# Kernel optimization log

Measured on AMD Instinct MI355X. Metric: run time of the kernel, lower is better.

Reference implementation:

```python
import jax, jax.numpy as jnp
import numpy as np

B, S, D, N = 4, 4096, 512, 512  # d_state must equal d_model for the original broadcast to be valid


def setup_inputs() -> dict:
    key = jax.random.key(0)
    ks = jax.random.split(key, 8)
    inv = 1.0 / np.sqrt(D)
    return {
        "x": jax.random.normal(ks[0], (B, S, D), dtype=jnp.float32),
        "state0": jnp.zeros((B, N), dtype=jnp.float32),
        "W_gate": (jax.random.normal(ks[1], (D, D)) * inv).astype(jnp.float32),  # x_proj_gate.weight [out,in]
        "b_gate": jnp.zeros((D,), jnp.float32),
        "W_sp": (jax.random.normal(ks[2], (N, D)) * inv).astype(jnp.float32),    # state_proj.weight [d_state, d_model]
        "b_sp": jnp.zeros((N,), jnp.float32),
        "W_out": (jax.random.normal(ks[3], (D, D)) * inv).astype(jnp.float32),   # out_proj.weight
        "b_out": jnp.zeros((D,), jnp.float32),
        "A_log": (jax.random.normal(ks[4], (D, N)) * 0.02).astype(jnp.float32),
        "D_param": jnp.ones((D,), jnp.float32),
    }


def reference(x, state0, W_gate, b_gate, W_sp, b_sp, W_out, b_out, A_log, D_param):
    # x_gate = silu(x_proj_gate(x))  [B,S,D]
    x_gate = jax.nn.silu(x @ W_gate.T + b_gate)
    # s = state_proj(x_gate)  [B,S,N]
    s = x_gate @ W_sp.T + b_sp
    # A = -exp(A_log); per-step decay = exp(mean_N(A))  [D] (== N by construction)
    A = -jnp.exp(A_log)
    decay = jnp.exp(A.mean(axis=-1))

    def step(state, s_t):  # state [B,N], s_t [B,N]
        state = state * decay + s_t
        return state, state

    state_f, states = jax.lax.scan(step, state0, jnp.swapaxes(s, 0, 1))  # states [S,B,N]
    # y_t = state_t @ state_proj.weight + D * u_t
    y = jnp.einsum('sbn,nd->bsd', states, W_sp) + D_param * x_gate
    out = y @ W_out.T + b_out  # out_proj
    return out, state_f
```

## Files before the change

kernel.cpp:

```cpp
#include <hip/hip_runtime.h>
#include <hip/hip_bf16.h>
#include <stdint.h>


typedef __bf16 bf16_t;
typedef bf16_t bf16x8 __attribute__((ext_vector_type(8)));
typedef bf16_t bf16x4 __attribute__((ext_vector_type(4)));
typedef float  f32x4  __attribute__((ext_vector_type(4)));

static __device__ __forceinline__ void async_copy16(bf16_t* lds, const bf16_t* g) {
    __builtin_amdgcn_global_load_lds((const __attribute__((address_space(1))) void*)g,
                                     (__attribute__((address_space(3))) void*)lds, 16, 0, 0);
}

template <int MODE, int NT>
__global__ __launch_bounds__(256, 2) void gemm_2ph(
    const bf16_t* __restrict__ A0, const bf16_t* __restrict__ W0,
    const bf16_t* __restrict__ A1, const bf16_t* __restrict__ W1,
    const float* __restrict__ bias, void* __restrict__ outp, int M)
{
    constexpr int K = 512;
    __shared__ bf16_t As[2][128 * 64];
    __shared__ bf16_t Bs[2][128 * 64];
    const int tid = threadIdx.x;
    int bid = blockIdx.x;
    {
        int nwg = gridDim.x;
        if ((nwg & 7) == 0) bid = (bid & 7) * (nwg >> 3) + (bid >> 3);
    }
    const int m0 = (bid >> 2) << 7, n0 = (bid & 3) << 7;
    const int l = tid & 63, w = tid >> 6;
    const int wr = w >> 1, wc = w & 1;
    const int lr = l & 15, kc = l >> 4;
    const int rloc = l >> 3, sc = (l & 7) ^ rloc;

    float bv[4];
    #pragma unroll
    for (int j = 0; j < 4; ++j)
        bv[j] = bias ? bias[n0 + wc * 64 + j * 16 + lr] : 0.f;

    f32x4 acc[4][4];
    const f32x4 z = {0.f, 0.f, 0.f, 0.f};
    #pragma unroll
    for (int i = 0; i < 4; ++i)
        #pragma unroll
        for (int j = 0; j < 4; ++j) acc[i][j] = z;

    auto stage = [&](int t) {
        const bf16_t* __restrict__ Asrc = (t < 8) ? A0 : A1;
        const bf16_t* __restrict__ Wsrc = (t < 8) ? W0 : W1;
        const int kk = (t & 7) << 6;
        bf16_t* bufA = As[t & 1];
        bf16_t* bufB = Bs[t & 1];
        #pragma unroll
        for (int v = 0; v < 4; ++v) {
            const int win = w * 4 + v;
            async_copy16(bufA + win * 512,
                         Asrc + (size_t)(m0 + win * 8 + rloc) * K + kk + sc * 8);
            async_copy16(bufB + win * 512,
                         Wsrc + (size_t)(n0 + win * 8 + rloc) * K + kk + sc * 8);
        }
    };

    stage(0);
    __syncthreads();

    #pragma unroll
    for (int t = 0; t < NT; ++t) {
        if (t + 1 < NT) stage(t + 1);
        const bf16_t* __restrict__ bufA = As[t & 1];
        const bf16_t* __restrict__ bufB = Bs[t & 1];
        bf16x8 a[2][4], b[2][4];
        #pragma unroll
        for (int ks = 0; ks < 2; ++ks) {
            #pragma unroll
            for (int i = 0; i < 4; ++i)
                a[ks][i] = *(const bf16x8*)(bufA + (wr * 64 + i * 16 + lr) * 64
                                            + (((ks * 4 + kc) ^ (lr & 7)) << 3));
            #pragma unroll
            for (int j = 0; j < 4; ++j)
                b[ks][j] = *(const bf16x8*)(bufB + (wc * 64 + j * 16 + lr) * 64
                                            + (((ks * 4 + kc) ^ (lr & 7)) << 3));
        }
        #pragma unroll
        for (int ks = 0; ks < 2; ++ks)
            #pragma unroll
            for (int i = 0; i < 4; ++i)
                #pragma unroll
                for (int j = 0; j < 4; ++j)
                    acc[i][j] = __builtin_amdgcn_mfma_f32_16x16x32_bf16(
                        a[ks][i], b[ks][j], acc[i][j], 0, 0, 0);
        if (t + 1 < NT) __syncthreads();
    }

    if (MODE == 0) {
        float* outF = (float*)outp;
        #pragma unroll
        for (int i = 0; i < 4; ++i) {
            const int row = m0 + wr * 64 + i * 16 + kc * 4;
            #pragma unroll
            for (int j = 0; j < 4; ++j) {
                const int col = n0 + wc * 64 + j * 16 + lr;
                #pragma unroll
                for (int r = 0; r < 4; ++r)
                    outF[(size_t)(row + r) * 512 + col] = acc[i][j][r] + bv[j];
            }
        }
    } else {
        __syncthreads();
        bf16_t* eps = &As[0][0];
        #pragma unroll
        for (int i = 0; i < 4; ++i) {
            const int row = wr * 64 + i * 16 + kc * 4;
            #pragma unroll
            for (int j = 0; j < 4; ++j) {
                const int col = wc * 64 + j * 16 + lr;
                #pragma unroll
                for (int r = 0; r < 4; ++r) {
                    float v = acc[i][j][r] + bv[j];
                    if (MODE == 2) v = v / (1.f + __expf(-v));
                    eps[(row + r) * 128 + col] = (bf16_t)v;
                }
            }
        }
        __syncthreads();
        bf16_t* outB = (bf16_t*)outp;
        #pragma unroll
        for (int s2 = 0; s2 < 8; ++s2) {
            const int row = s2 * 16 + (tid >> 4);
            const int col = (tid & 15) * 8;
            *(bf16x8*)(outB + (size_t)(m0 + row) * 512 + n0 + col) =
                *(const bf16x8*)(eps + row * 128 + col);
        }
    }
}

__global__ void prep_all(const float4* __restrict__ x, bf16x4* __restrict__ xb,
                         const float* __restrict__ Wg, const float* __restrict__ Wsp,
                         const float* __restrict__ Wo, const float* __restrict__ Dp,
                         bf16_t* __restrict__ Wg_bf, bf16_t* __restrict__ Wsp_bf,
                         bf16_t* __restrict__ Wo_bf, bf16_t* __restrict__ W2_bf,
                         const float* __restrict__ A_log, float* __restrict__ decay)
{
    const int blk = blockIdx.x, tid = threadIdx.x;
    {
        int i = blk * 256 + tid;
        float4 v = x[i];
        bf16x4 o;
        o[0] = (bf16_t)v.x; o[1] = (bf16_t)v.y; o[2] = (bf16_t)v.z; o[3] = (bf16_t)v.w;
        xb[i] = o;
    }
    if (blk < 1024) {
        int i = blk * 256 + tid;
        Wg_bf[i]  = (bf16_t)Wg[i];
        Wsp_bf[i] = (bf16_t)Wsp[i];
        float wo  = Wo[i];
        Wo_bf[i]  = (bf16_t)wo;
        W2_bf[i]  = (bf16_t)(wo * Dp[i & 511]);
    }
    if (blk < 128) {
        int d = blk * 4 + (tid >> 6);
        int ll = tid & 63;
        const float* row = A_log + (size_t)d * 512;
        float s = 0.f;
        for (int k = ll; k < 512; k += 64) s += expf(row[k]);
        #pragma unroll
        for (int off = 32; off > 0; off >>= 1) s += __shfl_down(s, off);
        if (ll == 0) decay[d] = expf(-s * (1.f / 512.f));
    }
}

__global__ void scan_partial(const bf16_t* __restrict__ s, const float* __restrict__ decay,
                             float* __restrict__ carry)
{
    int g = blockIdx.x * 256 + threadIdx.x;
    int n = g & 511, ch = (g >> 9) & 63, b = g >> 15;
    float dec = decay[n];
    const bf16_t* sp = s + (size_t)(b * 4096 + ch * 64) * 512 + n;
    float st = 0.f;
    #pragma unroll 8
    for (int i = 0; i < 64; ++i) st = st * dec + (float)sp[(size_t)i * 512];
    carry[(size_t)(b * 64 + ch) * 512 + n] = st;
}

__global__ void scan_carry(const float* __restrict__ carry, const float* __restrict__ decay,
                           const float* __restrict__ state0,
                           float* __restrict__ exc, float* __restrict__ state_f)
{
    int g = blockIdx.x * 256 + threadIdx.x;
    int n = g & 511, b = g >> 9;
    float dec = decay[n];
    float d64 = dec;
    #pragma unroll
    for (int t = 0; t < 6; ++t) d64 *= d64;
    float st = state0[g];
    for (int ch = 0; ch < 64; ++ch) {
        size_t idx = (size_t)(b * 64 + ch) * 512 + n;
        exc[idx] = st;
        st = st * d64 + carry[idx];
    }
    state_f[g] = st;
}

__global__ void scan_final(const bf16_t* __restrict__ s, const float* __restrict__ decay,
                           const float* __restrict__ exc, bf16_t* __restrict__ states)
{
    int g = blockIdx.x * 256 + threadIdx.x;
    int n = g & 511, ch = (g >> 9) & 63, b = g >> 15;
    float dec = decay[n];
    float st = exc[(size_t)(b * 64 + ch) * 512 + n];
    size_t base = (size_t)(b * 4096 + ch * 64) * 512 + n;
    #pragma unroll 8
    for (int i = 0; i < 64; ++i) {
        st = st * dec + (float)s[base + (size_t)i * 512];
        states[base + (size_t)i * 512] = (bf16_t)st;
    }
}

extern "C" void kernel_launch(void* const* d_in, const int* in_sizes, int n_in,
                              void* d_out, int out_size, void* d_ws, size_t ws_size,
                              hipStream_t stream)
{
    const float* x      = (const float*)d_in[0];
    const float* state0 = (const float*)d_in[1];
    const float* W_gate = (const float*)d_in[2];
    const float* b_gate = (const float*)d_in[3];
    const float* W_sp   = (const float*)d_in[4];
    const float* b_sp   = (const float*)d_in[5];
    const float* W_out  = (const float*)d_in[6];
    const float* b_out  = (const float*)d_in[7];
    const float* A_log  = (const float*)d_in[8];
    const float* D_par  = (const float*)d_in[9];
    float* out = (float*)d_out;

    char* ws = (char*)d_ws;
    bf16_t* x_bf   = (bf16_t*)ws;
    bf16_t* states = x_bf;
    bf16_t* xg_bf  = (bf16_t*)(ws + (16u << 20));
    bf16_t* s_bf   = (bf16_t*)(ws + (32u << 20));
    bf16_t* Wg_bf  = (bf16_t*)(ws + (48u << 20));
    bf16_t* Wsp_bf = Wg_bf + 262144;
    bf16_t* Wo_bf  = Wg_bf + 2 * 262144;
    bf16_t* W2_bf  = Wg_bf + 3 * 262144;
    bf16_t* WcT_bf = Wg_bf + 4 * 262144;
    float*  carry  = (float*)(Wg_bf + 5 * 262144);
    float*  exc    = carry + 131072;
    float*  decay  = exc + 131072;

    prep_all<<<dim3(8192), dim3(256), 0, stream>>>(
        (const float4*)x, (bf16x4*)x_bf, W_gate, W_sp, W_out, D_par,
        Wg_bf, Wsp_bf, Wo_bf, W2_bf, A_log, decay);

    gemm_2ph<1, 8><<<dim3(16), dim3(256), 0, stream>>>(
        Wo_bf, Wsp_bf, (const bf16_t*)nullptr, (const bf16_t*)nullptr,
        (const float*)nullptr, (void*)WcT_bf, 512);
    gemm_2ph<2, 8><<<dim3(512), dim3(256), 0, stream>>>(
        x_bf, Wg_bf, (const bf16_t*)nullptr, (const bf16_t*)nullptr,
        b_gate, (void*)xg_bf, 16384);
    gemm_2ph<1, 8><<<dim3(512), dim3(256), 0, stream>>>(
        xg_bf, Wsp_bf, (const bf16_t*)nullptr, (const bf16_t*)nullptr,
        b_sp, (void*)s_bf, 16384);

    scan_partial<<<dim3(512), dim3(256), 0, stream>>>(s_bf, decay, carry);
    scan_carry<<<dim3(8), dim3(256), 0, stream>>>(carry, decay, state0, exc, out + 8388608);
    scan_final<<<dim3(512), dim3(256), 0, stream>>>(s_bf, decay, exc, states);

    gemm_2ph<0, 16><<<dim3(512), dim3(256), 0, stream>>>(
        states, WcT_bf, xg_bf, W2_bf, b_out, (void*)out, 16384);
}
```

Baseline: 96.69 us.

## Fuse chunk-carry scan into state-proj GEMM epilogue and merge carry propagation

The state-projection GEMM now computes each 64-row chunk's partial scan carry directly from its LDS epilogue tile, which removes the separate scan_partial pass that re-read s from global memory. The carry-propagation kernel is dropped: each thread of the final scan replays the previous chunk carries itself, then writes the states and, for the last chunk, the final state. This saves two launches and a full read of s. In exchange the GEMM epilogue gets a serial 64-step loop and the final scan does up to 63 redundant carry steps per thread.

```diff
diff --git a/kernel.cpp b/kernel.cpp
--- a/kernel.cpp
+++ b/kernel.cpp
@@ -13,11 +13,12 @@
                                      (__attribute__((address_space(3))) void*)lds, 16, 0, 0);
 }
 
-template <int MODE, int NT>
+template <int MODE, int NT, bool SCAN>
 __global__ __launch_bounds__(256, 2) void gemm_2ph(
     const bf16_t* __restrict__ A0, const bf16_t* __restrict__ W0,
     const bf16_t* __restrict__ A1, const bf16_t* __restrict__ W1,
-    const float* __restrict__ bias, void* __restrict__ outp, int M)
+    const float* __restrict__ bias, void* __restrict__ outp,
+    const float* __restrict__ decay_g, float* __restrict__ carry_g)
 {
     constexpr int K = 512;
     __shared__ bf16_t As[2][128 * 64];
@@ -132,6 +133,16 @@
             *(bf16x8*)(outB + (size_t)(m0 + row) * 512 + n0 + col) =
                 *(const bf16x8*)(eps + row * 128 + col);
         }
+        if (SCAN) {
+            const int chalf = tid >> 7, col = tid & 127;
+            const int n = n0 + col;
+            const float dec = decay_g[n];
+            float st = 0.f;
+            #pragma unroll 8
+            for (int i = 0; i < 64; ++i)
+                st = st * dec + (float)eps[(chalf * 64 + i) * 128 + col];
+            carry_g[(size_t)((m0 >> 6) + chalf) * 512 + n] = st;
+        }
     }
 }
 
@@ -170,51 +181,27 @@
     }
 }
 
-__global__ void scan_partial(const bf16_t* __restrict__ s, const float* __restrict__ decay,
-                             float* __restrict__ carry)
+__global__ void scan_final2(const bf16_t* __restrict__ s, const float* __restrict__ decay,
+                            const float* __restrict__ carry, const float* __restrict__ state0,
+                            bf16_t* __restrict__ states, float* __restrict__ state_f)
 {
     int g = blockIdx.x * 256 + threadIdx.x;
     int n = g & 511, ch = (g >> 9) & 63, b = g >> 15;
     float dec = decay[n];
-    const bf16_t* sp = s + (size_t)(b * 4096 + ch * 64) * 512 + n;
-    float st = 0.f;
-    #pragma unroll 8
-    for (int i = 0; i < 64; ++i) st = st * dec + (float)sp[(size_t)i * 512];
-    carry[(size_t)(b * 64 + ch) * 512 + n] = st;
-}
-
-__global__ void scan_carry(const float* __restrict__ carry, const float* __restrict__ decay,
-                           const float* __restrict__ state0,
-                           float* __restrict__ exc, float* __restrict__ state_f)
-{
-    int g = blockIdx.x * 256 + threadIdx.x;
-    int n = g & 511, b = g >> 9;
-    float dec = decay[n];
     float d64 = dec;
     #pragma unroll
     for (int t = 0; t < 6; ++t) d64 *= d64;
-    float st = state0[g];
-    for (int ch = 0; ch < 64; ++ch) {
-        size_t idx = (size_t)(b * 64 + ch) * 512 + n;
-        exc[idx] = st;
-        st = st * d64 + carry[idx];
-    }
-    state_f[g] = st;
-}
-
-__global__ void scan_final(const bf16_t* __restrict__ s, const float* __restrict__ decay,
-                           const float* __restrict__ exc, bf16_t* __restrict__ states)
-{
-    int g = blockIdx.x * 256 + threadIdx.x;
-    int n = g & 511, ch = (g >> 9) & 63, b = g >> 15;
-    float dec = decay[n];
-    float st = exc[(size_t)(b * 64 + ch) * 512 + n];
+    float st = state0[b * 512 + n];
+    const float* crow = carry + (size_t)b * 64 * 512 + n;
+    for (int c = 0; c < ch; ++c)
+        st = st * d64 + crow[(size_t)c * 512];
     size_t base = (size_t)(b * 4096 + ch * 64) * 512 + n;
     #pragma unroll 8
     for (int i = 0; i < 64; ++i) {
         st = st * dec + (float)s[base + (size_t)i * 512];
         states[base + (size_t)i * 512] = (bf16_t)st;
     }
+    if (ch == 63) state_f[b * 512 + n] = st;
 }
 
 extern "C" void kernel_launch(void* const* d_in, const int* in_sizes, int n_in,
@@ -244,27 +231,26 @@
     bf16_t* W2_bf  = Wg_bf + 3 * 262144;
     bf16_t* WcT_bf = Wg_bf + 4 * 262144;
     float*  carry  = (float*)(Wg_bf + 5 * 262144);
-    float*  exc    = carry + 131072;
-    float*  decay  = exc + 131072;
+    float*  decay  = carry + 131072;
 
     prep_all<<<dim3(8192), dim3(256), 0, stream>>>(
         (const float4*)x, (bf16x4*)x_bf, W_gate, W_sp, W_out, D_par,
         Wg_bf, Wsp_bf, Wo_bf, W2_bf, A_log, decay);
 
-    gemm_2ph<1, 8><<<dim3(16), dim3(256), 0, stream>>>(
+    gemm_2ph<1, 8, false><<<dim3(16), dim3(256), 0, stream>>>(
         Wo_bf, Wsp_bf, (const bf16_t*)nullptr, (const bf16_t*)nullptr,
-        (const float*)nullptr, (void*)WcT_bf, 512);
-    gemm_2ph<2, 8><<<dim3(512), dim3(256), 0, stream>>>(
+        (const float*)nullptr, (void*)WcT_bf, (const float*)nullptr, (float*)nullptr);
+    gemm_2ph<2, 8, false><<<dim3(512), dim3(256), 0, stream>>>(
         x_bf, Wg_bf, (const bf16_t*)nullptr, (const bf16_t*)nullptr,
-        b_gate, (void*)xg_bf, 16384);
-    gemm_2ph<1, 8><<<dim3(512), dim3(256), 0, stream>>>(
+        b_gate, (void*)xg_bf, (const float*)nullptr, (float*)nullptr);
+    gemm_2ph<1, 8, true><<<dim3(512), dim3(256), 0, stream>>>(
         xg_bf, Wsp_bf, (const bf16_t*)nullptr, (const bf16_t*)nullptr,
-        b_sp, (void*)s_bf, 16384);
-
-    scan_partial<<<dim3(512), dim3(256), 0, stream>>>(s_bf, decay, carry);
-    scan_carry<<<dim3(8), dim3(256), 0, stream>>>(carry, decay, state0, exc, out + 8388608);
-    scan_final<<<dim3(512), dim3(256), 0, stream>>>(s_bf, decay, exc, states);
-
-    gemm_2ph<0, 16><<<dim3(512), dim3(256), 0, stream>>>(
-        states, WcT_bf, xg_bf, W2_bf, b_out, (void*)out, 16384);
-}
+        b_sp, (void*)s_bf, decay, carry);
+
+    scan_final2<<<dim3(512), dim3(256), 0, stream>>>(
+        s_bf, decay, carry, state0, states, out + 8388608);
+
+    gemm_2ph<0, 16, false><<<dim3(512), dim3(256), 0, stream>>>(
+        states, WcT_bf, xg_bf, W2_bf, b_out, (void*)out,
+        (const float*)nullptr, (float*)nullptr);
+}
```

Measured after the change: 104.2 us. +7.8%, slower.
